# Optimization experiments

Measured on AMD Instinct MI355X. Metric: run time of the kernel, lower is better.

Reference implementation:

```python
import jax, jax.numpy as jnp
import numpy as np

B, S, C, H = 8, 1024, 768, 8
D = C // H  # head dim = 96
MLP = 4 * C


def setup_inputs() -> dict:
    key = jax.random.key(0)
    ks = jax.random.split(key, 12)
    sc = 0.02
    return {
        "x": jax.random.normal(ks[0], (B, S, C), jnp.float32),
        "ln1_w": jnp.ones((S, C), jnp.float32),
        "ln1_b": jnp.zeros((S, C), jnp.float32),
        "ln2_w": jnp.ones((S, C), jnp.float32),
        "ln2_b": jnp.zeros((S, C), jnp.float32),
        "qkv_w": jax.random.normal(ks[1], (C, 3 * C), jnp.float32) * sc,
        "proj_w": jax.random.normal(ks[2], (C, C), jnp.float32) * sc,
        "mlp_w1": jax.random.normal(ks[3], (C, MLP), jnp.float32) * sc,
        "mlp_b1": jnp.zeros((MLP,), jnp.float32),
        "mlp_w2": jax.random.normal(ks[4], (MLP, C), jnp.float32) * sc,
        "mlp_b2": jnp.zeros((C,), jnp.float32),
    }


def _layernorm2d(x, w, b, eps=1e-5):
    # normalizes over BOTH (seq, channel) dims, per nn.LayerNorm([length, channel])
    mu = jnp.mean(x, axis=(-2, -1), keepdims=True)
    var = jnp.mean(jnp.square(x - mu), axis=(-2, -1), keepdims=True)
    return (x - mu) * jax.lax.rsqrt(var + eps) * w + b


def _attention(x, qkv_w, proj_w):
    b, s, _ = x.shape
    qkv = (x @ qkv_w).reshape(b, s, 3, H, D)
    q, k, v = qkv[:, :, 0], qkv[:, :, 1], qkv[:, :, 2]  # [b, s, h, d]
    # NOTE: original module applies NO 1/sqrt(d) scaling
    scores = jnp.einsum("bshd,bthd->bhst", q, k)
    attn = jax.nn.softmax(scores, axis=-1)
    out = jnp.einsum("bhst,bthd->bshd", attn, v).reshape(b, s, C)
    return out @ proj_w


def reference(x, ln1_w, ln1_b, ln2_w, ln2_b, qkv_w, proj_w, mlp_w1, mlp_b1, mlp_w2, mlp_b2):
    # dropout is identity in eval mode
    h = x + _attention(_layernorm2d(x, ln1_w, ln1_b), qkv_w, proj_w)
    y = _layernorm2d(h, ln2_w, ln2_b)
    y = jax.nn.gelu(y @ mlp_w1 + mlp_b1, approximate=False)
    return h + (y @ mlp_w2 + mlp_b2)
```

## Files before the change

kernel.cpp:

```cpp
#include <hip/hip_runtime.h>
#include <hip/hip_bf16.h>

#define S_LEN 1024
#define NB 8
#define NC 768
#define NH 8
#define HD 96
#define NMLP 3072
#define SC (S_LEN*NC)
#define BS (NB*S_LEN)

typedef __attribute__((ext_vector_type(8))) unsigned short u16x8;
typedef __attribute__((ext_vector_type(4))) unsigned short u16x4;
typedef __attribute__((ext_vector_type(8))) __bf16 bf16x8;
typedef __attribute__((ext_vector_type(4))) float f32x4;

__device__ __forceinline__ unsigned short f2b(float f) {
  union { __hip_bfloat16 h; unsigned short u; } cvt;
  cvt.h = __float2bfloat16(f);
  return cvt.u;
}

__device__ __forceinline__ void gload16(const unsigned short* g, unsigned short* l) {
  __builtin_amdgcn_global_load_lds(
      (const __attribute__((address_space(1))) unsigned int*)g,
      (__attribute__((address_space(3))) unsigned int*)l, 16, 0, 0);
}

__device__ __forceinline__ float gelu_f(float v) {
  float u = v * (0.7978845608f + 0.0356774081f * v * v);
  float au = fabsf(u);
  float e = __expf(-2.0f * au);
  float th = (1.0f - e) / (1.0f + e);
  th = copysignf(th, u);
  return 0.5f * v * (1.0f + th);
}

template<int EPI>
__global__ __launch_bounds__(512, 1)
void gemm8(const unsigned short* __restrict__ A, int lda,
           const unsigned short* __restrict__ Bt, int ldb,
           void* __restrict__ Cv, int ldc, int K,
           const float* __restrict__ bias,
           const float* __restrict__ residual, int ldr,
           float* __restrict__ lnred)
{
  __shared__ unsigned short As[3*16384];
  __shared__ unsigned short Bs[3*8192];
  const int tid = threadIdx.x, lane = tid & 63, wid = tid >> 6;
  const int wm = wid & 3, wn = wid >> 2;
  const int r15 = lane & 15, g = lane >> 4;
  const int tm = blockIdx.x * 256, tn = blockIdx.y * 128;
  const int NT = K >> 6;

  const int srow = lane >> 3;
  const int scol = ((lane & 7) ^ srow) << 3;
  const unsigned short* Ag = A  + (size_t)(tm + wid*32 + srow)*lda + scol;
  const unsigned short* Bg = Bt + (size_t)(tn + wid*16 + srow)*ldb + scol;

  const int kx  = (r15 & 7) << 4;
  const int k0b = (g*16) ^ kx;
  const int k1b = (64 + g*16) ^ kx;
  char* AsB = (char*)As;
  char* BsB = (char*)Bs;
  const int arow = (wm*64 + r15) * 128;
  const int brow = (wn*64 + r15) * 128;

#define LDA8(m,ks) (*(const bf16x8*)(AsB + bufA + arow + (m)*2048 + ((ks) ? k1b : k0b)))
#define LDB8(n,ks) (*(const bf16x8*)(BsB + bufB + brow + (n)*2048 + ((ks) ? k1b : k0b)))
#define STGA(i,kk,bf) gload16(Ag + (size_t)((i)*8)*lda + (kk), As + (bf)*16384 + (wid*4 + (i))*512)
#define STGB(i,kk,bf) gload16(Bg + (size_t)((i)*8)*ldb + (kk), Bs + (bf)*8192  + (wid*2 + (i))*512)
#define MFMA16(a8,b8,c) __builtin_amdgcn_mfma_f32_16x16x32_bf16(a8, b8, c, 0, 0, 0)
#define SBAR() __builtin_amdgcn_sched_barrier(0)

  f32x4 acc[4][4];
  #pragma unroll
  for (int m = 0; m < 4; ++m)
    #pragma unroll
    for (int n = 0; n < 4; ++n)
      acc[m][n] = (f32x4){0.f, 0.f, 0.f, 0.f};

  STGA(0,0,0); STGA(1,0,0); STGA(2,0,0); STGA(3,0,0); STGB(0,0,0); STGB(1,0,0);
  STGA(0,64,1); STGA(1,64,1); STGA(2,64,1); STGA(3,64,1); STGB(0,64,1); STGB(1,64,1);
  asm volatile("s_waitcnt vmcnt(6)" ::: "memory");
  __builtin_amdgcn_s_barrier();

  int buf = 0, nbuf = 2;
  for (int t = 0; t < NT; ++t) {
    const int kk = (t + 2) << 6;
    const bool pre = (t + 2) < NT;
    const int bufA = buf * 32768;
    const int bufB = buf * 16384;
    bf16x8 a[4][2], b0[2][2], b1[2][2];

    #pragma unroll
    for (int m = 0; m < 4; ++m) { a[m][0] = LDA8(m,0); a[m][1] = LDA8(m,1); }
    #pragma unroll
    for (int n = 0; n < 2; ++n) { b0[n][0] = LDB8(n,0); b0[n][1] = LDB8(n,1); }
    if (pre) { STGA(0,kk,nbuf); STGA(1,kk,nbuf); STGB(0,kk,nbuf); }
    SBAR();
    __builtin_amdgcn_s_barrier();
    asm volatile("s_waitcnt lgkmcnt(0)" ::: "memory");
    SBAR();
    __builtin_amdgcn_s_setprio(1);
    #pragma unroll
    for (int m = 0; m < 4; ++m)
      #pragma unroll
      for (int n = 0; n < 2; ++n) {
        acc[m][n] = MFMA16(a[m][0], b0[n][0], acc[m][n]);
        acc[m][n] = MFMA16(a[m][1], b0[n][1], acc[m][n]);
      }
    __builtin_amdgcn_s_setprio(0);
    SBAR();
    __builtin_amdgcn_s_barrier();

    #pragma unroll
    for (int n = 0; n < 2; ++n) { b1[n][0] = LDB8(n+2,0); b1[n][1] = LDB8(n+2,1); }
    if (pre) { STGA(2,kk,nbuf); STGA(3,kk,nbuf); STGB(1,kk,nbuf); }
    SBAR();
    __builtin_amdgcn_s_barrier();
    asm volatile("s_waitcnt lgkmcnt(0)" ::: "memory");
    SBAR();
    __builtin_amdgcn_s_setprio(1);
    #pragma unroll
    for (int m = 0; m < 4; ++m)
      #pragma unroll
      for (int n = 0; n < 2; ++n) {
        acc[m][n+2] = MFMA16(a[m][0], b1[n][0], acc[m][n+2]);
        acc[m][n+2] = MFMA16(a[m][1], b1[n][1], acc[m][n+2]);
      }
    __builtin_amdgcn_s_setprio(0);
    SBAR();
    if (pre) asm volatile("s_waitcnt vmcnt(6)" ::: "memory");
    else     asm volatile("s_waitcnt vmcnt(0)" ::: "memory");
    __builtin_amdgcn_s_barrier();
    buf  = (buf  == 2) ? 0 : buf  + 1;
    nbuf = (nbuf == 2) ? 0 : nbuf + 1;
  }
#undef LDA8
#undef LDB8
#undef STGA
#undef STGB
#undef MFMA16
#undef SBAR

  unsigned short* Cu = (unsigned short*)Cv;
  float* Cf = (float*)Cv;
  float s1 = 0.f, s2 = 0.f;
  #pragma unroll
  for (int m = 0; m < 4; ++m) {
    #pragma unroll
    for (int n = 0; n < 4; ++n) {
      const int col = tn + wn*64 + n*16 + r15;
      #pragma unroll
      for (int r = 0; r < 4; ++r) {
        const int row = tm + wm*64 + m*16 + g*4 + r;
        float v = acc[m][n][r];
        if (EPI == 2 || EPI == 4) v += bias[col];
        if (EPI == 3 || EPI == 4) v += residual[(size_t)row*ldr + col];
        if (EPI == 2) v = gelu_f(v);
        if (EPI == 3) { s1 += v; s2 += v*v; }
        if (EPI == 0 || EPI == 2) Cu[(size_t)row*ldc + col] = f2b(v);
        else                      Cf[(size_t)row*ldc + col] = v;
      }
    }
  }
  if (EPI == 3) {
    #pragma unroll
    for (int o = 32; o; o >>= 1) { s1 += __shfl_xor(s1, o); s2 += __shfl_xor(s2, o); }
    __syncthreads();
    float* red = (float*)As;
    if (lane == 0) { red[wid*2] = s1; red[wid*2+1] = s2; }
    __syncthreads();
    if (tid == 0) {
      float a1 = 0.f, a2 = 0.f;
      #pragma unroll
      for (int w = 0; w < 8; ++w) { a1 += red[w*2]; a2 += red[w*2+1]; }
      const int bidx = tm >> 10;
      atomicAdd(&lnred[bidx*2],     a1);
      atomicAdd(&lnred[bidx*2 + 1], a2);
    }
  }
}

__global__ __launch_bounds__(256, 2)
void flash_attn(const unsigned short* __restrict__ qkv,
                const unsigned short* __restrict__ vt,
                unsigned short* __restrict__ outb)
{
  __shared__ unsigned short Ks[128*96];
  __shared__ unsigned short Vs[96*128];
  __shared__ unsigned short Ps[128*128];
  const int tid = threadIdx.x, lane = tid & 63, wq = tid >> 6;
  const int r15 = lane & 15, g = lane >> 4;
  const int bh = blockIdx.y, b = bh >> 3, h = bh & 7;
  const int q0 = blockIdx.x * 128;
  const int swz = (r15 & 7) << 4;
  char* PsB = (char*)Ps;
  char* VsB = (char*)Vs;

  bf16x8 qf[2][3];
  {
    const unsigned short* qb = qkv + ((size_t)b*S_LEN + q0 + wq*32 + r15)*2304 + h*HD + g*8;
    #pragma unroll
    for (int n = 0; n < 2; ++n)
      #pragma unroll
      for (int kc = 0; kc < 3; ++kc)
        qf[n][kc] = *(const bf16x8*)(qb + (size_t)n*16*2304 + kc*32);
  }

  int krow[6], kcol[6], vrow[6], vcol[6];
  #pragma unroll
  for (int i = 0; i < 6; ++i) {
    const int c = (wq*6 + i)*64 + lane;
    krow[i] = c / 12;
    kcol[i] = (c % 12) * 8;
    const int L = c * 16;
    const int row = L >> 8, cb = L & 255;
    vrow[i] = row;
    vcol[i] = (cb ^ ((row & 7) << 4)) >> 1;
  }
  const unsigned short* kbase = qkv + (size_t)b*S_LEN*2304 + NC + h*HD;
  const unsigned short* vbase = vt + (size_t)bh*HD*S_LEN;

  f32x4 oacc[6][2];
  #pragma unroll
  for (int m = 0; m < 6; ++m) {
    oacc[m][0] = (f32x4){0.f,0.f,0.f,0.f};
    oacc[m][1] = (f32x4){0.f,0.f,0.f,0.f};
  }
  float mrun[2] = {-INFINITY, -INFINITY};
  float lrun[2] = {0.f, 0.f};

  for (int kt = 0; kt < 8; ++kt) {
    const unsigned short* ksrc = kbase + (size_t)kt*128*2304;
    const unsigned short* vsrc = vbase + kt*128;
    #pragma unroll
    for (int i = 0; i < 6; ++i) {
      gload16(ksrc + (size_t)krow[i]*2304 + kcol[i], Ks + (wq*6 + i)*512);
      gload16(vsrc + vrow[i]*1024 + vcol[i],         Vs + (wq*6 + i)*512);
    }
    __syncthreads();

    f32x4 sacc[8][2];
    #pragma unroll
    for (int m = 0; m < 8; ++m) {
      sacc[m][0] = (f32x4){0.f,0.f,0.f,0.f};
      sacc[m][1] = (f32x4){0.f,0.f,0.f,0.f};
    }
    __builtin_amdgcn_s_setprio(1);
    #pragma unroll
    for (int kc = 0; kc < 3; ++kc)
      #pragma unroll
      for (int m = 0; m < 8; ++m) {
        bf16x8 kf = *(const bf16x8*)(Ks + (m*16 + r15)*96 + kc*32 + g*8);
        sacc[m][0] = __builtin_amdgcn_mfma_f32_16x16x32_bf16(kf, qf[0][kc], sacc[m][0], 0,0,0);
        sacc[m][1] = __builtin_amdgcn_mfma_f32_16x16x32_bf16(kf, qf[1][kc], sacc[m][1], 0,0,0);
      }
    __builtin_amdgcn_s_setprio(0);

    #pragma unroll
    for (int n = 0; n < 2; ++n) {
      float pm = -INFINITY;
      #pragma unroll
      for (int m = 0; m < 8; ++m)
        #pragma unroll
        for (int r = 0; r < 4; ++r) pm = fmaxf(pm, sacc[m][n][r]);
      pm = fmaxf(pm, __shfl_xor(pm, 16));
      pm = fmaxf(pm, __shfl_xor(pm, 32));
      const float newm = fmaxf(mrun[n], pm);
      const float scale = __expf(mrun[n] - newm);
      mrun[n] = newm;
      const int qloc = wq*32 + n*16 + r15;
      float s = 0.f;
      #pragma unroll
      for (int m = 0; m < 8; ++m) {
        float e0 = __expf(sacc[m][n][0] - newm);
        float e1 = __expf(sacc[m][n][1] - newm);
        float e2 = __expf(sacc[m][n][2] - newm);
        float e3 = __expf(sacc[m][n][3] - newm);
        s += (e0 + e1) + (e2 + e3);
        u16x4 pk = { f2b(e0), f2b(e1), f2b(e2), f2b(e3) };
        *(u16x4*)(PsB + ((qloc*256 + m*32 + g*8) ^ swz)) = pk;
      }
      s += __shfl_xor(s, 16);
      s += __shfl_xor(s, 32);
      lrun[n] = lrun[n]*scale + s;
      #pragma unroll
      for (int m = 0; m < 6; ++m) oacc[m][n] *= scale;
    }

    #pragma unroll
    for (int kc = 0; kc < 4; ++kc) {
      bf16x8 pf0 = *(const bf16x8*)(PsB + (((wq*32      + r15)*256 + kc*64 + g*16) ^ swz));
      bf16x8 pf1 = *(const bf16x8*)(PsB + (((wq*32 + 16 + r15)*256 + kc*64 + g*16) ^ swz));
      __builtin_amdgcn_s_setprio(1);
      #pragma unroll
      for (int m = 0; m < 6; ++m) {
        bf16x8 vf = *(const bf16x8*)(VsB + (((m*16 + r15)*256 + kc*64 + g*16) ^ swz));
        oacc[m][0] = __builtin_amdgcn_mfma_f32_16x16x32_bf16(vf, pf0, oacc[m][0], 0,0,0);
        oacc[m][1] = __builtin_amdgcn_mfma_f32_16x16x32_bf16(vf, pf1, oacc[m][1], 0,0,0);
      }
      __builtin_amdgcn_s_setprio(0);
    }
    __syncthreads();
  }

  #pragma unroll
  for (int n = 0; n < 2; ++n) {
    const float inv = 1.0f / lrun[n];
    unsigned short* orow = outb + ((size_t)b*S_LEN + q0 + wq*32 + n*16 + r15)*NC + h*HD;
    #pragma unroll
    for (int m = 0; m < 6; ++m) {
      u16x4 pk = { f2b(oacc[m][n][0]*inv), f2b(oacc[m][n][1]*inv),
                   f2b(oacc[m][n][2]*inv), f2b(oacc[m][n][3]*inv) };
      *(u16x4*)(orow + m*16 + g*4) = pk;
    }
  }
}

__global__ void transpose_cast(const float* __restrict__ W, unsigned short* __restrict__ Wt,
                               int K, int N)
{
  __shared__ float tile[32][33];
  const int tx = threadIdx.x & 31, ty = threadIdx.x >> 5;
  const int n0 = blockIdx.x * 32, k0 = blockIdx.y * 32;
  #pragma unroll
  for (int i = 0; i < 32; i += 8)
    tile[ty + i][tx] = W[(size_t)(k0 + ty + i)*N + n0 + tx];
  __syncthreads();
  #pragma unroll
  for (int i = 0; i < 32; i += 8)
    Wt[(size_t)(n0 + ty + i)*K + k0 + tx] = f2b(tile[tx][ty + i]);
}

__global__ void transpose_v(const unsigned short* __restrict__ qkv, unsigned short* __restrict__ vt)
{
  __shared__ unsigned short tile[32][33];
  const int bh = blockIdx.z, b = bh >> 3, h = bh & 7;
  const unsigned short* v = qkv + (size_t)b*S_LEN*3*NC + 2*NC + h*HD;
  unsigned short* o = vt + (size_t)bh*HD*S_LEN;
  const int s0 = blockIdx.x * 32, d0 = blockIdx.y * 32;
  const int tx = threadIdx.x & 31, ty = threadIdx.x >> 5;
  #pragma unroll
  for (int i = 0; i < 32; i += 8)
    tile[ty + i][tx] = v[(size_t)(s0 + ty + i)*(3*NC) + d0 + tx];
  __syncthreads();
  #pragma unroll
  for (int i = 0; i < 32; i += 8)
    o[(size_t)(d0 + ty + i)*S_LEN + s0 + tx] = tile[tx][ty + i];
}

__global__ void ln_part(const float* __restrict__ X, float* __restrict__ part)
{
  const int b = blockIdx.x / 96, blk = blockIdx.x % 96;
  const float4* xb = (const float4*)(X + (size_t)b*SC);
  float s = 0.f, s2 = 0.f;
  #pragma unroll
  for (int i = 0; i < 8; ++i) {
    float4 v = xb[blk*2048 + i*256 + threadIdx.x];
    s  += v.x + v.y + v.z + v.w;
    s2 += v.x*v.x + v.y*v.y + v.z*v.z + v.w*v.w;
  }
  #pragma unroll
  for (int o = 32; o; o >>= 1) { s += __shfl_down(s, o); s2 += __shfl_down(s2, o); }
  __shared__ float r1[4], r2[4];
  const int w = threadIdx.x >> 6;
  if ((threadIdx.x & 63) == 0) { r1[w] = s; r2[w] = s2; }
  __syncthreads();
  if (threadIdx.x == 0) {
    part[(b*96 + blk)*2]     = r1[0] + r1[1] + r1[2] + r1[3];
    part[(b*96 + blk)*2 + 1] = r2[0] + r2[1] + r2[2] + r2[3];
  }
}

__global__ void ln_fin(const float* __restrict__ part, float* __restrict__ stats)
{
  const int b = blockIdx.x;
  float s = 0.f, s2 = 0.f;
  for (int i = threadIdx.x; i < 96; i += 64) {
    s  += part[(b*96 + i)*2];
    s2 += part[(b*96 + i)*2 + 1];
  }
  #pragma unroll
  for (int o = 32; o; o >>= 1) { s += __shfl_down(s, o); s2 += __shfl_down(s2, o); }
  if (threadIdx.x == 0) {
    const float inv = 1.0f / (float)SC;
    const float mu = s * inv;
    const float var = s2 * inv - mu*mu;
    stats[b*2] = mu;
    stats[b*2 + 1] = rsqrtf(var + 1e-5f);
  }
}

__global__ void ln_apply(const float* __restrict__ X, const float* __restrict__ W,
                         const float* __restrict__ Bv, const float* __restrict__ stats,
                         unsigned short* __restrict__ out)
{
  const size_t i = ((size_t)blockIdx.x*256 + threadIdx.x) * 8;
  const int b = (int)(i / SC);
  const size_t r = i % SC;
  const float mu = stats[b*2], rs = stats[b*2 + 1];
  float4 x0 = *(const float4*)(X + i),  x1 = *(const float4*)(X + i + 4);
  float4 w0 = *(const float4*)(W + r),  w1 = *(const float4*)(W + r + 4);
  float4 b0 = *(const float4*)(Bv + r), b1 = *(const float4*)(Bv + r + 4);
  u16x8 o;
  o[0] = f2b((x0.x - mu)*rs*w0.x + b0.x);
  o[1] = f2b((x0.y - mu)*rs*w0.y + b0.y);
  o[2] = f2b((x0.z - mu)*rs*w0.z + b0.z);
  o[3] = f2b((x0.w - mu)*rs*w0.w + b0.w);
  o[4] = f2b((x1.x - mu)*rs*w1.x + b1.x);
  o[5] = f2b((x1.y - mu)*rs*w1.y + b1.y);
  o[6] = f2b((x1.z - mu)*rs*w1.z + b1.z);
  o[7] = f2b((x1.w - mu)*rs*w1.w + b1.w);
  *(u16x8*)(out + i) = o;
}

__global__ void ln_apply_f(const float* __restrict__ X, const float* __restrict__ W,
                           const float* __restrict__ Bv, const float* __restrict__ red,
                           unsigned short* __restrict__ out)
{
  const size_t i = ((size_t)blockIdx.x*256 + threadIdx.x) * 8;
  const int b = (int)(i / SC);
  const size_t r = i % SC;
  const float inv = 1.0f / (float)SC;
  const float mu = red[b*2] * inv;
  const float var = red[b*2 + 1] * inv - mu*mu;
  const float rs = rsqrtf(var + 1e-5f);
  float4 x0 = *(const float4*)(X + i),  x1 = *(const float4*)(X + i + 4);
  float4 w0 = *(const float4*)(W + r),  w1 = *(const float4*)(W + r + 4);
  float4 b0 = *(const float4*)(Bv + r), b1 = *(const float4*)(Bv + r + 4);
  u16x8 o;
  o[0] = f2b((x0.x - mu)*rs*w0.x + b0.x);
  o[1] = f2b((x0.y - mu)*rs*w0.y + b0.y);
  o[2] = f2b((x0.z - mu)*rs*w0.z + b0.z);
  o[3] = f2b((x0.w - mu)*rs*w0.w + b0.w);
  o[4] = f2b((x1.x - mu)*rs*w1.x + b1.x);
  o[5] = f2b((x1.y - mu)*rs*w1.y + b1.y);
  o[6] = f2b((x1.z - mu)*rs*w1.z + b1.z);
  o[7] = f2b((x1.w - mu)*rs*w1.w + b1.w);
  *(u16x8*)(out + i) = o;
}

extern "C" void kernel_launch(void* const* d_in, const int* in_sizes, int n_in,
                              void* d_out, int out_size, void* d_ws, size_t ws_size,
                              hipStream_t stream) {
  const float* x      = (const float*)d_in[0];
  const float* ln1_w  = (const float*)d_in[1];
  const float* ln1_b  = (const float*)d_in[2];
  const float* ln2_w  = (const float*)d_in[3];
  const float* ln2_b  = (const float*)d_in[4];
  const float* qkv_w  = (const float*)d_in[5];
  const float* proj_w = (const float*)d_in[6];
  const float* mlp_w1 = (const float*)d_in[7];
  const float* mlp_b1 = (const float*)d_in[8];
  const float* mlp_w2 = (const float*)d_in[9];
  const float* mlp_b2 = (const float*)d_in[10];
  float* out = (float*)d_out;

  char* ws = (char*)d_ws;
  size_t off = 0;
  auto alloc = [&](size_t b) { size_t o = off; off += (b + 255) & ~(size_t)255; return o; };
  unsigned short* wqkvT  = (unsigned short*)(ws + alloc((size_t)3*NC*NC*2));
  unsigned short* wprojT = (unsigned short*)(ws + alloc((size_t)NC*NC*2));
  unsigned short* w1T    = (unsigned short*)(ws + alloc((size_t)NMLP*NC*2));
  unsigned short* w2T    = (unsigned short*)(ws + alloc((size_t)NC*NMLP*2));
  unsigned short* lnbf   = (unsigned short*)(ws + alloc((size_t)BS*NC*2));
  const size_t qkvOff    = alloc((size_t)BS*3*NC*2);
  unsigned short* qkvbf  = (unsigned short*)(ws + qkvOff);
  unsigned short* vt     = (unsigned short*)(ws + alloc((size_t)NB*NH*HD*S_LEN*2));
  unsigned short* ybf    = (unsigned short*)(ws + qkvOff);
  float* hbuf            = (float*)(ws + alloc((size_t)BS*NC*4));
  float* part            = (float*)(ws + alloc((size_t)NB*96*2*4));
  float* stats           = (float*)(ws + alloc((size_t)NB*2*4));
  float* lnred           = (float*)(ws + alloc((size_t)NB*2*4));
  (void)ws_size; (void)in_sizes; (void)n_in; (void)out_size;

  const dim3 blk(256);
  const dim3 blk512(512);

  hipMemsetAsync(lnred, 0, NB*2*sizeof(float), stream);

  transpose_cast<<<dim3(3*NC/32, NC/32),   blk, 0, stream>>>(qkv_w,  wqkvT,  NC, 3*NC);
  transpose_cast<<<dim3(NC/32, NC/32),     blk, 0, stream>>>(proj_w, wprojT, NC, NC);
  transpose_cast<<<dim3(NMLP/32, NC/32),   blk, 0, stream>>>(mlp_w1, w1T,    NC, NMLP);
  transpose_cast<<<dim3(NC/32, NMLP/32),   blk, 0, stream>>>(mlp_w2, w2T,    NMLP, NC);

  ln_part<<<dim3(NB*96), blk, 0, stream>>>(x, part);
  ln_fin<<<dim3(NB), dim3(64), 0, stream>>>(part, stats);
  ln_apply<<<dim3(BS*NC/2048), blk, 0, stream>>>(x, ln1_w, ln1_b, stats, lnbf);

  gemm8<0><<<dim3(BS/256, 3*NC/128), blk512, 0, stream>>>(
      lnbf, NC, wqkvT, NC, qkvbf, 3*NC, NC, nullptr, nullptr, 0, nullptr);

  transpose_v<<<dim3(S_LEN/32, HD/32, NB*NH), blk, 0, stream>>>(qkvbf, vt);

  flash_attn<<<dim3(S_LEN/128, NB*NH), blk, 0, stream>>>(qkvbf, vt, lnbf);

  gemm8<3><<<dim3(BS/256, NC/128), blk512, 0, stream>>>(
      lnbf, NC, wprojT, NC, hbuf, NC, NC, nullptr, x, NC, lnred);

  ln_apply_f<<<dim3(BS*NC/2048), blk, 0, stream>>>(hbuf, ln2_w, ln2_b, lnred, lnbf);

  gemm8<2><<<dim3(BS/256, NMLP/128), blk512, 0, stream>>>(
      lnbf, NC, w1T, NC, ybf, NMLP, NC, mlp_b1, nullptr, 0, nullptr);

  gemm8<4><<<dim3(BS/256, NC/128), blk512, 0, stream>>>(
      ybf, NMLP, w2T, NMLP, out, NC, NMLP, mlp_b2, hbuf, NC, nullptr);
}
```

Baseline: 284.9 us.

## Fuse V transpose into QKV GEMM epilogue and merge small launches

The QKV GEMM gains an epilogue that writes the Q and K columns as before but stores the V columns directly in the transposed per-head layout the attention kernel expects, which removes the separate transpose_v pass. The four weight transpose-cast launches are merged into one kernel with a flat block index. The first layernorm's partial, finalize and apply kernels are replaced by an atomic sum kernel plus the existing ln_apply_f. The goal is fewer launches and less global memory traffic, at the cost of scattered 8-byte V stores in the GEMM epilogue and atomic contention on 16 floats.

Result: no change. 290.4 us (+1.9%).

```diff
diff --git a/kernel.cpp b/kernel.cpp
--- a/kernel.cpp
+++ b/kernel.cpp
@@ -43,7 +43,8 @@
            void* __restrict__ Cv, int ldc, int K,
            const float* __restrict__ bias,
            const float* __restrict__ residual, int ldr,
-           float* __restrict__ lnred)
+           float* __restrict__ lnred,
+           unsigned short* __restrict__ vtout)
 {
   __shared__ unsigned short As[3*16384];
   __shared__ unsigned short Bs[3*8192];
@@ -152,6 +153,7 @@
     #pragma unroll
     for (int n = 0; n < 4; ++n) {
       const int col = tn + wn*64 + n*16 + r15;
+      float vv[4];
       #pragma unroll
       for (int r = 0; r < 4; ++r) {
         const int row = tm + wm*64 + m*16 + g*4 + r;
@@ -160,8 +162,24 @@
         if (EPI == 3 || EPI == 4) v += residual[(size_t)row*ldr + col];
         if (EPI == 2) v = gelu_f(v);
         if (EPI == 3) { s1 += v; s2 += v*v; }
+        vv[r] = v;
+        if (EPI == 5) continue;
         if (EPI == 0 || EPI == 2) Cu[(size_t)row*ldc + col] = f2b(v);
         else                      Cf[(size_t)row*ldc + col] = v;
+      }
+      if (EPI == 5) {
+        const int row0 = tm + wm*64 + m*16 + g*4;
+        if (col < 1536) {
+          #pragma unroll
+          for (int r = 0; r < 4; ++r)
+            Cu[(size_t)(row0 + r)*ldc + col] = f2b(vv[r]);
+        } else {
+          const int vg = col - 1536;
+          const int h = vg / HD, d = vg % HD;
+          const int b = row0 >> 10, s = row0 & 1023;
+          u16x4 pk = { f2b(vv[0]), f2b(vv[1]), f2b(vv[2]), f2b(vv[3]) };
+          *(u16x4*)(vtout + ((size_t)((b*NH + h)*HD + d) << 10) + s) = pk;
+        }
       }
     }
   }
@@ -319,12 +337,25 @@
   }
 }
 
-__global__ void transpose_cast(const float* __restrict__ W, unsigned short* __restrict__ Wt,
-                               int K, int N)
+__global__ void transpose_cast_all(const float* __restrict__ qkv_w,
+                                   const float* __restrict__ proj_w,
+                                   const float* __restrict__ w1,
+                                   const float* __restrict__ w2,
+                                   unsigned short* __restrict__ wqkvT,
+                                   unsigned short* __restrict__ wprojT,
+                                   unsigned short* __restrict__ w1T,
+                                   unsigned short* __restrict__ w2T)
 {
+  int id = blockIdx.x;
+  const float* W; unsigned short* Wt; int K, N, nx;
+  if (id < 1728)      {            W = qkv_w;  Wt = wqkvT;  K = NC;   N = 3*NC;  nx = 72; }
+  else if (id < 2304) { id -= 1728; W = proj_w; Wt = wprojT; K = NC;   N = NC;    nx = 24; }
+  else if (id < 4608) { id -= 2304; W = w1;     Wt = w1T;    K = NC;   N = NMLP;  nx = 96; }
+  else                { id -= 4608; W = w2;     Wt = w2T;    K = NMLP; N = NC;    nx = 24; }
+  const int n0 = (id % nx) * 32, k0 = (id / nx) * 32;
+
   __shared__ float tile[32][33];
   const int tx = threadIdx.x & 31, ty = threadIdx.x >> 5;
-  const int n0 = blockIdx.x * 32, k0 = blockIdx.y * 32;
   #pragma unroll
   for (int i = 0; i < 32; i += 8)
     tile[ty + i][tx] = W[(size_t)(k0 + ty + i)*N + n0 + tx];
@@ -334,24 +365,7 @@
     Wt[(size_t)(n0 + ty + i)*K + k0 + tx] = f2b(tile[tx][ty + i]);
 }
 
-__global__ void transpose_v(const unsigned short* __restrict__ qkv, unsigned short* __restrict__ vt)
-{
-  __shared__ unsigned short tile[32][33];
-  const int bh = blockIdx.z, b = bh >> 3, h = bh & 7;
-  const unsigned short* v = qkv + (size_t)b*S_LEN*3*NC + 2*NC + h*HD;
-  unsigned short* o = vt + (size_t)bh*HD*S_LEN;
-  const int s0 = blockIdx.x * 32, d0 = blockIdx.y * 32;
-  const int tx = threadIdx.x & 31, ty = threadIdx.x >> 5;
-  #pragma unroll
-  for (int i = 0; i < 32; i += 8)
-    tile[ty + i][tx] = v[(size_t)(s0 + ty + i)*(3*NC) + d0 + tx];
-  __syncthreads();
-  #pragma unroll
-  for (int i = 0; i < 32; i += 8)
-    o[(size_t)(d0 + ty + i)*S_LEN + s0 + tx] = tile[tx][ty + i];
-}
-
-__global__ void ln_part(const float* __restrict__ X, float* __restrict__ part)
+__global__ void ln_sum(const float* __restrict__ X, float* __restrict__ red)
 {
   const int b = blockIdx.x / 96, blk = blockIdx.x % 96;
   const float4* xb = (const float4*)(X + (size_t)b*SC);
@@ -369,51 +383,9 @@
   if ((threadIdx.x & 63) == 0) { r1[w] = s; r2[w] = s2; }
   __syncthreads();
   if (threadIdx.x == 0) {
-    part[(b*96 + blk)*2]     = r1[0] + r1[1] + r1[2] + r1[3];
-    part[(b*96 + blk)*2 + 1] = r2[0] + r2[1] + r2[2] + r2[3];
-  }
-}
-
-__global__ void ln_fin(const float* __restrict__ part, float* __restrict__ stats)
-{
-  const int b = blockIdx.x;
-  float s = 0.f, s2 = 0.f;
-  for (int i = threadIdx.x; i < 96; i += 64) {
-    s  += part[(b*96 + i)*2];
-    s2 += part[(b*96 + i)*2 + 1];
-  }
-  #pragma unroll
-  for (int o = 32; o; o >>= 1) { s += __shfl_down(s, o); s2 += __shfl_down(s2, o); }
-  if (threadIdx.x == 0) {
-    const float inv = 1.0f / (float)SC;
-    const float mu = s * inv;
-    const float var = s2 * inv - mu*mu;
-    stats[b*2] = mu;
-    stats[b*2 + 1] = rsqrtf(var + 1e-5f);
-  }
-}
-
-__global__ void ln_apply(const float* __restrict__ X, const float* __restrict__ W,
-                         const float* __restrict__ Bv, const float* __restrict__ stats,
-                         unsigned short* __restrict__ out)
-{
-  const size_t i = ((size_t)blockIdx.x*256 + threadIdx.x) * 8;
-  const int b = (int)(i / SC);
-  const size_t r = i % SC;
-  const float mu = stats[b*2], rs = stats[b*2 + 1];
-  float4 x0 = *(const float4*)(X + i),  x1 = *(const float4*)(X + i + 4);
-  float4 w0 = *(const float4*)(W + r),  w1 = *(const float4*)(W + r + 4);
-  float4 b0 = *(const float4*)(Bv + r), b1 = *(const float4*)(Bv + r + 4);
-  u16x8 o;
-  o[0] = f2b((x0.x - mu)*rs*w0.x + b0.x);
-  o[1] = f2b((x0.y - mu)*rs*w0.y + b0.y);
-  o[2] = f2b((x0.z - mu)*rs*w0.z + b0.z);
-  o[3] = f2b((x0.w - mu)*rs*w0.w + b0.w);
-  o[4] = f2b((x1.x - mu)*rs*w1.x + b1.x);
-  o[5] = f2b((x1.y - mu)*rs*w1.y + b1.y);
-  o[6] = f2b((x1.z - mu)*rs*w1.z + b1.z);
-  o[7] = f2b((x1.w - mu)*rs*w1.w + b1.w);
-  *(u16x8*)(out + i) = o;
+    atomicAdd(&red[b*2],     r1[0] + r1[1] + r1[2] + r1[3]);
+    atomicAdd(&red[b*2 + 1], r2[0] + r2[1] + r2[2] + r2[3]);
+  }
 }
 
 __global__ void ln_apply_f(const float* __restrict__ X, const float* __restrict__ W,
@@ -471,40 +443,36 @@
   unsigned short* vt     = (unsigned short*)(ws + alloc((size_t)NB*NH*HD*S_LEN*2));
   unsigned short* ybf    = (unsigned short*)(ws + qkvOff);
   float* hbuf            = (float*)(ws + alloc((size_t)BS*NC*4));
-  float* part            = (float*)(ws + alloc((size_t)NB*96*2*4));
-  float* stats           = (float*)(ws + alloc((size_t)NB*2*4));
-  float* lnred           = (float*)(ws + alloc((size_t)NB*2*4));
+  float* lnred           = (float*)(ws + alloc((size_t)4*NB*4));
   (void)ws_size; (void)in_sizes; (void)n_in; (void)out_size;
+
+  float* red1 = lnred;
+  float* red2 = lnred + 2*NB;
 
   const dim3 blk(256);
   const dim3 blk512(512);
 
-  hipMemsetAsync(lnred, 0, NB*2*sizeof(float), stream);
-
-  transpose_cast<<<dim3(3*NC/32, NC/32),   blk, 0, stream>>>(qkv_w,  wqkvT,  NC, 3*NC);
-  transpose_cast<<<dim3(NC/32, NC/32),     blk, 0, stream>>>(proj_w, wprojT, NC, NC);
-  transpose_cast<<<dim3(NMLP/32, NC/32),   blk, 0, stream>>>(mlp_w1, w1T,    NC, NMLP);
-  transpose_cast<<<dim3(NC/32, NMLP/32),   blk, 0, stream>>>(mlp_w2, w2T,    NMLP, NC);
-
-  ln_part<<<dim3(NB*96), blk, 0, stream>>>(x, part);
-  ln_fin<<<dim3(NB), dim3(64), 0, stream>>>(part, stats);
-  ln_apply<<<dim3(BS*NC/2048), blk, 0, stream>>>(x, ln1_w, ln1_b, stats, lnbf);
-
-  gemm8<0><<<dim3(BS/256, 3*NC/128), blk512, 0, stream>>>(
-      lnbf, NC, wqkvT, NC, qkvbf, 3*NC, NC, nullptr, nullptr, 0, nullptr);
-
-  transpose_v<<<dim3(S_LEN/32, HD/32, NB*NH), blk, 0, stream>>>(qkvbf, vt);
+  hipMemsetAsync(lnred, 0, 4*NB*sizeof(float), stream);
+
+  transpose_cast_all<<<dim3(6912), blk, 0, stream>>>(
+      qkv_w, proj_w, mlp_w1, mlp_w2, wqkvT, wprojT, w1T, w2T);
+
+  ln_sum<<<dim3(NB*96), blk, 0, stream>>>(x, red1);
+  ln_apply_f<<<dim3(BS*NC/2048), blk, 0, stream>>>(x, ln1_w, ln1_b, red1, lnbf);
+
+  gemm8<5><<<dim3(BS/256, 3*NC/128), blk512, 0, stream>>>(
+      lnbf, NC, wqkvT, NC, qkvbf, 3*NC, NC, nullptr, nullptr, 0, nullptr, vt);
 
   flash_attn<<<dim3(S_LEN/128, NB*NH), blk, 0, stream>>>(qkvbf, vt, lnbf);
 
   gemm8<3><<<dim3(BS/256, NC/128), blk512, 0, stream>>>(
-      lnbf, NC, wprojT, NC, hbuf, NC, NC, nullptr, x, NC, lnred);
-
-  ln_apply_f<<<dim3(BS*NC/2048), blk, 0, stream>>>(hbuf, ln2_w, ln2_b, lnred, lnbf);
+      lnbf, NC, wprojT, NC, hbuf, NC, NC, nullptr, x, NC, red2, nullptr);
+
+  ln_apply_f<<<dim3(BS*NC/2048), blk, 0, stream>>>(hbuf, ln2_w, ln2_b, red2, lnbf);
 
   gemm8<2><<<dim3(BS/256, NMLP/128), blk512, 0, stream>>>(
-      lnbf, NC, w1T, NC, ybf, NMLP, NC, mlp_b1, nullptr, 0, nullptr);
+      lnbf, NC, w1T, NC, ybf, NMLP, NC, mlp_b1, nullptr, 0, nullptr, nullptr);
 
   gemm8<4><<<dim3(BS/256, NC/128), blk512, 0, stream>>>(
-      ybf, NMLP, w2T, NMLP, out, NC, NMLP, mlp_b2, hbuf, NC, nullptr);
-}
+      ybf, NMLP, w2T, NMLP, out, NC, NMLP, mlp_b2, hbuf, NC, nullptr, nullptr);
+}
```
